# Kernel optimization log

Measured on AMD Instinct MI355X. Metric: run time of the kernel, lower is better.

The kernel has to match this reference:

```python
import jax, jax.numpy as jnp
import numpy as np

# Module hyperparameters (from init_kwargs)
KH, KW = 3, 3        # kernel_size
SH, SW = 1, 1        # stride
PH, PW = 1, 1        # padding
NUM_ITER = 3         # num_iterations


def squash(t, axis=-1):
    # scale = |t|^2 / (1 + |t|^2); out = scale * t / |t|
    sq = jnp.sum(t * t, axis=axis, keepdims=True)
    return (sq / (1.0 + sq)) * t / jnp.sqrt(sq)


def setup_inputs() -> dict:
    key = jax.random.key(0)
    k1, k2 = jax.random.split(key)
    x = jax.random.normal(k1, (4, 32, 56, 56), dtype=jnp.float32)
    # weight: (P_out, P_in, K, L_in, L_out) = (64//16, 32//8, 3*3, 8, 16)
    # (the original stores an extra size-1 dim at position 2; squeezed here)
    weight = jax.random.normal(k2, (4, 4, 9, 8, 16), dtype=jnp.float32)
    return {"x": x, "weight": weight}


def reference(x, weight):
    N, C_in, H, W = x.shape
    P_out, P_in, K, L_in, L_out = weight.shape
    H_out = (H + 2 * PH - KH) // SH + 1
    W_out = (W + 2 * PW - KW) // SW + 1

    # im2col: (N, C_in, H_out, W_out, K)
    xp = jnp.pad(x, ((0, 0), (0, 0), (PH, PH), (PW, PW)))
    patches = jnp.stack(
        [xp[:, :, dj:dj + SH * H_out:SH, dk:dk + SW * W_out:SW]
         for dj in range(KH) for dk in range(KW)],
        axis=-1,
    )
    # split channels into capsule planes: (N, P_in, L_in, H_out, W_out, K)
    patches = patches.reshape(N, P_in, L_in, H_out, W_out, K)

    # priors[n,o,p,h,w,k,:] = window[n,p,h,w,k,:] @ weight[o,p,k,:,:]
    priors = jnp.einsum('nplhwk,opkld->nophwkd', patches, weight)

    # dynamic routing. logits broadcast over the L_out dim in the original
    # (delta_logits has a keepdim size-1 last axis), so track them as (...,K,1).
    logits = jnp.zeros(priors.shape[:-1] + (1,), priors.dtype)
    outputs = None
    for i in range(NUM_ITER):
        probs = jax.nn.softmax(logits, axis=-2)          # softmax over K
        s = jnp.sum(probs * priors, axis=-2, keepdims=True)  # (...,1,L_out)
        outputs = squash(s, axis=-1)
        if i != NUM_ITER - 1:
            logits = logits + jnp.sum(priors * outputs, axis=-1, keepdims=True)

    # sum routed outputs over input capsule planes (the .add accumulation)
    out = jnp.sum(outputs[..., 0, :], axis=2)            # (N, P_out, H_out, W_out, L_out)
    out = jnp.transpose(out, (0, 1, 4, 2, 3)).reshape(N, P_out * L_out, H_out, W_out)
    return out
```

## Files before the change

### kernel.cpp

```cpp
#include <hip/hip_runtime.h>


#define HW 56
#define HW2 3136
#define WSTRIDE 1168

__device__ __forceinline__ float quad_add1(float x) {
    int y = __builtin_amdgcn_update_dpp(0, __float_as_int(x), 0xB1, 0xF, 0xF, true);
    return x + __int_as_float(y);
}
__device__ __forceinline__ float quad_add2(float x) {
    int y = __builtin_amdgcn_update_dpp(0, __float_as_int(x), 0x4E, 0xF, 0xF, true);
    return x + __int_as_float(y);
}
__device__ __forceinline__ float quad_reduce(float x) {
    return quad_add2(quad_add1(x));
}

__global__ void caps_routing_kernel(
    const float* __restrict__ x, const float* __restrict__ wgt,
    float* __restrict__ out)
{
    __shared__ float lds_w[4 * WSTRIDE];

    const int tid = threadIdx.x;
    const int bx  = blockIdx.x;
    const int n = bx >> 2, o = bx & 3;

    {
        const float4* wsrc = (const float4*)(wgt + o * 4608);
        for (int i = tid; i < 1152; i += 256) {
            const int pp  = i / 288;
            const int rem = i - pp * 288;
            *(float4*)&lds_w[pp * WSTRIDE + rem * 4] = wsrc[i];
        }
    }
    __syncthreads();

    const int dq = tid & 3;
    const int wl = (tid >> 2) & 3;
    const int p  = (tid >> 4) & 3;

    const int t  = blockIdx.y * 4 + (tid >> 6);
    const int hp = t / 14;
    const int w0 = (t - hp * 14) * 4;
    const int h0 = hp * 2;

    float M[9][4][2];
    #pragma unroll
    for (int k = 0; k < 9; ++k)
        #pragma unroll
        for (int j = 0; j < 4; ++j) { M[k][j][0] = 0.f; M[k][j][1] = 0.f; }

    const float* xp = x + (n * 32 + p * 8) * HW2;
    const float* wbase = &lds_w[p * WSTRIDE + dq * 4];
    const int colbase = w0 + wl - 1;

    #pragma clang loop unroll(disable)
    for (int l = 0; l < 8; ++l) {
        float xv[4][3];
        const float* xplane = xp + l * HW2;
        #pragma unroll
        for (int rr = 0; rr < 4; ++rr) {
            const int row = h0 + rr - 1;
            const bool rv = (unsigned)row < (unsigned)HW;
            const float* xrow = xplane + row * HW;
            #pragma unroll
            for (int c = 0; c < 3; ++c) {
                const int col = colbase + c;
                xv[rr][c] = (rv && (unsigned)col < (unsigned)HW) ? xrow[col] : 0.f;
            }
        }
        #pragma unroll
        for (int rr = 0; rr < 3; ++rr) {
            #pragma unroll
            for (int kc = 0; kc < 3; ++kc) {
                const int k = rr * 3 + kc;
                const float4 wa = *(const float4*)(wbase + (k * 8 + l) * 16);
                const float xs0 = xv[rr][kc];
                const float xs1 = xv[rr + 1][kc];
                M[k][0][0] += xs0 * wa.x; M[k][1][0] += xs0 * wa.y;
                M[k][2][0] += xs0 * wa.z; M[k][3][0] += xs0 * wa.w;
                M[k][0][1] += xs1 * wa.x; M[k][1][1] += xs1 * wa.y;
                M[k][2][1] += xs1 * wa.z; M[k][3][1] += xs1 * wa.w;
            }
        }
    }

    #pragma unroll
    for (int ti = 0; ti < 2; ++ti) {
        float v[4], b[9];
        {
            float s[4];
            #pragma unroll
            for (int j = 0; j < 4; ++j) {
                float a = M[0][j][ti];
                #pragma unroll
                for (int k = 1; k < 9; ++k) a += M[k][j][ti];
                s[j] = a * (1.f / 9.f);
            }
            float sq = s[0]*s[0] + s[1]*s[1] + s[2]*s[2] + s[3]*s[3];
            sq = quad_reduce(sq);
            const float scale = sq * __builtin_amdgcn_rsqf(sq) * __builtin_amdgcn_rcpf(1.f + sq);
            #pragma unroll
            for (int j = 0; j < 4; ++j) v[j] = s[j] * scale;
            #pragma unroll
            for (int k = 0; k < 9; ++k) {
                float u = M[k][0][ti]*v[0] + M[k][1][ti]*v[1]
                        + M[k][2][ti]*v[2] + M[k][3][ti]*v[3];
                b[k] = quad_reduce(u);
            }
        }

        #pragma unroll
        for (int it = 1; it < 3; ++it) {
            float mx = b[0];
            #pragma unroll
            for (int k = 1; k < 9; ++k) mx = fmaxf(mx, b[k]);
            float e[9]; float se = 0.f;
            #pragma unroll
            for (int k = 0; k < 9; ++k) { e[k] = __expf(b[k] - mx); se += e[k]; }
            const float inv = __builtin_amdgcn_rcpf(se);
            float s[4];
            #pragma unroll
            for (int j = 0; j < 4; ++j) {
                float a = 0.f;
                #pragma unroll
                for (int k = 0; k < 9; ++k) a += e[k] * M[k][j][ti];
                s[j] = a * inv;
            }
            float sq = s[0]*s[0] + s[1]*s[1] + s[2]*s[2] + s[3]*s[3];
            sq = quad_reduce(sq);
            const float scale = sq * __builtin_amdgcn_rsqf(sq) * __builtin_amdgcn_rcpf(1.f + sq);
            #pragma unroll
            for (int j = 0; j < 4; ++j) v[j] = s[j] * scale;
            if (it == 1) {
                #pragma unroll
                for (int k = 0; k < 9; ++k) {
                    float u = M[k][0][ti]*v[0] + M[k][1][ti]*v[1]
                            + M[k][2][ti]*v[2] + M[k][3][ti]*v[3];
                    b[k] += quad_reduce(u);
                }
            }
        }

        #pragma unroll
        for (int j = 0; j < 4; ++j) {
            v[j] += __shfl_xor(v[j], 16, 64);
            v[j] += __shfl_xor(v[j], 32, 64);
        }
        if (p == 0) {
            float* op = out + ((n * 64 + o * 16 + dq * 4) * HW + (h0 + ti)) * HW + w0 + wl;
            #pragma unroll
            for (int j = 0; j < 4; ++j) op[j * HW2] = v[j];
        }
    }
}

extern "C" void kernel_launch(void* const* d_in, const int* in_sizes, int n_in,
                              void* d_out, int out_size, void* d_ws, size_t ws_size,
                              hipStream_t stream) {
    const float* x   = (const float*)d_in[0];
    const float* wgt = (const float*)d_in[1];
    float* out = (float*)d_out;

    caps_routing_kernel<<<dim3(16, 98), dim3(256), 0, stream>>>(x, wgt, out);
}
```

Baseline: 77.97 us.

## Stage padded input tile in LDS and remap waves to 4x8 spatial tiles

Each block now covers a 4x8 output tile and cooperatively loads the padded 6x10 halo for all 32 input channels into LDS. The layout is channel-minor with a stride of 33 to avoid bank conflicts. The inner loop then reads from shared memory without per-element bounds checks, where before each thread made redundant global loads. The cost is extra LDS use per block, which may lower occupancy, plus an extra staging phase before the barrier.

Result: no change. 79.07 us (+1.4%).

```diff
diff --git a/kernel.cpp b/kernel.cpp
--- a/kernel.cpp
+++ b/kernel.cpp
@@ -4,6 +4,8 @@
 #define HW 56
 #define HW2 3136
 #define WSTRIDE 1168
+#define XSTR 33
+#define XN (60 * XSTR)
 
 __device__ __forceinline__ float quad_add1(float x) {
     int y = __builtin_amdgcn_update_dpp(0, __float_as_int(x), 0xB1, 0xF, 0xF, true);
@@ -22,10 +24,17 @@
     float* __restrict__ out)
 {
     __shared__ float lds_w[4 * WSTRIDE];
+    __shared__ float lds_x[XN];
 
     const int tid = threadIdx.x;
     const int bx  = blockIdx.x;
     const int n = bx >> 2, o = bx & 3;
+
+    const int by = blockIdx.y;
+    const int hb = by / 7;
+    const int wb = by - hb * 7;
+    const int h0 = hb * 4;
+    const int w0 = wb * 8;
 
     {
         const float4* wsrc = (const float4*)(wgt + o * 4608);
@@ -35,16 +44,28 @@
             *(float4*)&lds_w[pp * WSTRIDE + rem * 4] = wsrc[i];
         }
     }
+    {
+        const float* xn = x + n * 32 * HW2;
+        for (int idx = tid; idx < 1920; idx += 256) {
+            const int ch  = idx / 60;
+            const int rem = idx - ch * 60;
+            const int r   = rem / 10;
+            const int c   = rem - r * 10;
+            const int gr  = h0 - 1 + r;
+            const int gc  = w0 - 1 + c;
+            float v = 0.f;
+            if ((unsigned)gr < (unsigned)HW && (unsigned)gc < (unsigned)HW)
+                v = xn[ch * HW2 + gr * HW + gc];
+            lds_x[rem * XSTR + ch] = v;
+        }
+    }
     __syncthreads();
 
     const int dq = tid & 3;
     const int wl = (tid >> 2) & 3;
     const int p  = (tid >> 4) & 3;
-
-    const int t  = blockIdx.y * 4 + (tid >> 6);
-    const int hp = t / 14;
-    const int w0 = (t - hp * 14) * 4;
-    const int h0 = hp * 2;
+    const int wi = tid >> 6;
+    const int hh = wi >> 1, ww = wi & 1;
 
     float M[9][4][2];
     #pragma unroll
@@ -52,31 +73,25 @@
         #pragma unroll
         for (int j = 0; j < 4; ++j) { M[k][j][0] = 0.f; M[k][j][1] = 0.f; }
 
-    const float* xp = x + (n * 32 + p * 8) * HW2;
-    const float* wbase = &lds_w[p * WSTRIDE + dq * 4];
-    const int colbase = w0 + wl - 1;
+    const float* xb  = &lds_x[((hh * 2) * 10 + ww * 4 + wl) * XSTR + p * 8];
+    const float* wbp = &lds_w[p * WSTRIDE + dq * 4];
 
     #pragma clang loop unroll(disable)
     for (int l = 0; l < 8; ++l) {
+        const float* xl  = xb + l;
+        const float* wlp = wbp + l * 16;
         float xv[4][3];
-        const float* xplane = xp + l * HW2;
         #pragma unroll
-        for (int rr = 0; rr < 4; ++rr) {
-            const int row = h0 + rr - 1;
-            const bool rv = (unsigned)row < (unsigned)HW;
-            const float* xrow = xplane + row * HW;
+        for (int rr = 0; rr < 4; ++rr)
             #pragma unroll
-            for (int c = 0; c < 3; ++c) {
-                const int col = colbase + c;
-                xv[rr][c] = (rv && (unsigned)col < (unsigned)HW) ? xrow[col] : 0.f;
-            }
-        }
+            for (int c = 0; c < 3; ++c)
+                xv[rr][c] = xl[(rr * 10 + c) * XSTR];
         #pragma unroll
         for (int rr = 0; rr < 3; ++rr) {
             #pragma unroll
             for (int kc = 0; kc < 3; ++kc) {
                 const int k = rr * 3 + kc;
-                const float4 wa = *(const float4*)(wbase + (k * 8 + l) * 16);
+                const float4 wa = *(const float4*)(wlp + k * 128);
                 const float xs0 = xv[rr][kc];
                 const float xs1 = xv[rr + 1][kc];
                 M[k][0][0] += xs0 * wa.x; M[k][1][0] += xs0 * wa.y;
@@ -150,7 +165,8 @@
             v[j] += __shfl_xor(v[j], 32, 64);
         }
         if (p == 0) {
-            float* op = out + ((n * 64 + o * 16 + dq * 4) * HW + (h0 + ti)) * HW + w0 + wl;
+            float* op = out + ((n * 64 + o * 16 + dq * 4) * HW + (h0 + hh * 2 + ti)) * HW
+                      + w0 + ww * 4 + wl;
             #pragma unroll
             for (int j = 0; j < 4; ++j) op[j * HW2] = v[j];
         }
```
